# Optimization experiments

Measured on AMD Instinct MI355X. Metric: run time of the kernel, lower is better.

The kernel has to match this reference:

```python
import jax, jax.numpy as jnp
import numpy as np

# loss weights (match init_kwargs)
L_M, L_U, L_B, L_D = 1.0, 7.0, 2.0, 1.0
NV, NP, NI, NB = 500_000, 64, 48, 2  # voxels, predictions, instances, batches


def setup_inputs() -> dict:
    key = jax.random.key(0)
    k1, k2 = jax.random.split(key)
    logits = jax.random.normal(k1, (NV, NP), dtype=jnp.float32)
    # sorted batch ids per voxel (first half batch 0, second half batch 1)
    voxel_batch = (jnp.arange(NV) * NB // NV).astype(jnp.int32)
    per_b = NI // NB
    # instance ids consistent with voxel batch (module assumes one batch per instance)
    gt_ids = (voxel_batch * per_b + jax.random.randint(k2, (NV,), 0, per_b)).astype(jnp.int32)
    centroid_batches = (jnp.arange(NP) * NB // NP).astype(jnp.int32)
    return {"logits": logits, "voxel_batch": voxel_batch, "gt_ids": gt_ids,
            "centroid_batches": centroid_batches}


def linear_sum_assignment(cost):
    """Hungarian algorithm (e-maxx JV variant) on a small numpy cost matrix."""
    cost = np.asarray(cost, dtype=np.float64)
    transposed = cost.shape[0] > cost.shape[1]
    C = cost.T if transposed else cost
    n, m = C.shape
    u = np.zeros(n + 1); v = np.zeros(m + 1)
    p = np.zeros(m + 1, dtype=np.int64); way = np.zeros(m + 1, dtype=np.int64)
    for i in range(1, n + 1):
        p[0] = i; j0 = 0
        minv = np.full(m + 1, np.inf); used = np.zeros(m + 1, dtype=bool)
        while True:
            used[j0] = True
            i0 = p[j0]; j1 = 0; delta = np.inf
            for j in range(1, m + 1):
                if not used[j]:
                    cur = C[i0 - 1, j - 1] - u[i0] - v[j]
                    if cur < minv[j]:
                        minv[j] = cur; way[j] = j0
                    if minv[j] < delta:
                        delta = minv[j]; j1 = j
            for j in range(m + 1):
                if used[j]:
                    u[p[j]] += delta; v[j] -= delta
                else:
                    minv[j] -= delta
            j0 = j1
            if p[j0] == 0:
                break
        while j0:
            j1 = way[j0]; p[j0] = p[j1]; j0 = j1
    ans = np.zeros(n, dtype=np.int64)
    for j in range(1, m + 1):
        if p[j] > 0:
            ans[p[j] - 1] = j - 1
    rows, cols = np.arange(n), ans
    if transposed:
        rows, cols = cols, rows
    order = np.argsort(rows)
    return rows[order], cols[order]


def reference(logits, voxel_batch, gt_ids, centroid_batches):
    vb = np.asarray(voxel_batch); gi = np.asarray(gt_ids); cb = np.asarray(centroid_batches)
    batches = np.unique(vb)
    uniq, inv = np.unique(gi, return_inverse=True)
    uniq_batches = np.zeros(uniq.size, dtype=np.int64)
    uniq_batches[inv] = vb  # batch id per unique GT instance
    losses = jnp.zeros(5, dtype=logits.dtype)
    for b in batches:
        vox = np.nonzero(vb == b)[0]
        pidx = np.nonzero(cb == b)[0]
        gidx = np.nonzero(uniq_batches == b)[0]
        if pidx.size == 0:
            continue
        x = logits[jnp.asarray(vox)][:, jnp.asarray(pidx)].T          # [P, Nv_b]
        g = (jnp.asarray(gi[vox])[None, :] == jnp.asarray(uniq[gidx])[:, None]).astype(logits.dtype)  # [G, Nv_b]
        # matcher pairwise costs (mean BCE + dice)
        pos = jnp.logaddexp(0.0, -x)  # BCE(x, 1) per element
        neg = jnp.logaddexp(0.0, x)   # BCE(x, 0) per element
        nvb = x.shape[1]
        cost_bce = (pos @ g.T + neg @ (1.0 - g).T) / nvb              # [P, G]
        p = jax.nn.sigmoid(x)
        cost_dice = 1.0 - (2.0 * (p @ g.T) + 1.0) / (p.sum(1)[:, None] + g.sum(1)[None, :] + 1.0)
        cost = L_B * cost_bce + L_D * cost_dice
        pr, gr = linear_sum_assignment(np.asarray(cost))
        G = g.shape[0]
        xm = x[jnp.asarray(pr)]; gm = g[jnp.asarray(gr)]              # matched pairs
        bce = L_B * (jnp.logaddexp(0.0, xm) - xm * gm).mean(1).sum() / G
        pm = jax.nn.sigmoid(xm)
        dice = L_D * (1.0 - (2.0 * (pm * gm).sum(1) + 1.0) / (pm.sum(1) + gm.sum(1) + 1.0)).sum() / G
        matched = L_M * (bce + dice)
        um = np.setdiff1d(np.arange(x.shape[0]), pr)
        if um.size:
            xu = x[jnp.asarray(um)]
            pu = jax.nn.sigmoid(xu)
            # sigmoid focal loss vs zeros: alpha_t=0.75, (1-p_t)^2 = p^2, ce = softplus(x)
            unmatched = L_U * (0.75 * jnp.logaddexp(0.0, xu) * pu * pu).mean()
        else:
            unmatched = jnp.zeros((), logits.dtype)
        total = matched + unmatched
        losses = losses + jnp.stack([total, matched, unmatched, bce, dice])
    return losses / batches.size  # [total, matched, unmatched, bce, dice]
```

## Files before the change

### kernel.cpp

```cpp
#include <hip/hip_runtime.h>
#include <math.h>

#define PB 32
#define GB 24
#define NBUK 48
#define NH 256
#define SL 16
#define PART 160

__global__ __launch_bounds__(256) void k_hist(const int* __restrict__ gi, int NV,
                                              int* __restrict__ counts)
{
    __shared__ int h[NBUK];
    int t = threadIdx.x;
    if (t < NBUK) h[t] = 0;
    __syncthreads();
    int CH = (NV + NH - 1) / NH;
    int lo = blockIdx.x * CH, hi = lo + CH; if (hi > NV) hi = NV;
    for (int i = lo + t; i < hi; i += 256) atomicAdd(&h[gi[i]], 1);
    __syncthreads();
    if (t < NBUK) counts[t * NH + blockIdx.x] = h[t];
}

__global__ __launch_bounds__(1024) void k_scan(const int* __restrict__ counts,
                                               int* __restrict__ offs, int* __restrict__ bs)
{
    __shared__ int tot[NBUK];
    __shared__ int bstart[NBUK + 1];
    int t = threadIdx.x, w = t >> 6, lane = t & 63;
    int c[3][4]; int excl[3];
    #pragma unroll
    for (int q = 0; q < 3; ++q) {
        int g = w * 3 + q;
        int base = g * NH + lane * 4;
        int s = 0;
        #pragma unroll
        for (int j = 0; j < 4; ++j) { c[q][j] = counts[base + j]; s += c[q][j]; }
        int inc = s;
        for (int off = 1; off < 64; off <<= 1) {
            int v = __shfl_up(inc, off);
            if (lane >= off) inc += v;
        }
        excl[q] = inc - s;
        int rt = __shfl(inc, 63);
        if (lane == 0) tot[g] = rt;
    }
    __syncthreads();
    if (t == 0) {
        int acc = 0;
        for (int g = 0; g < NBUK; ++g) { bstart[g] = acc; acc += tot[g]; }
        bstart[NBUK] = acc;
        for (int g = 0; g <= NBUK; ++g) bs[g] = bstart[g];
    }
    __syncthreads();
    #pragma unroll
    for (int q = 0; q < 3; ++q) {
        int g = w * 3 + q;
        int run = excl[q] + bstart[g];
        #pragma unroll
        for (int j = 0; j < 4; ++j) { offs[g * NH + lane * 4 + j] = run; run += c[q][j]; }
    }
}

__global__ __launch_bounds__(256) void k_scatter(const int* __restrict__ gi, int NV,
                                                 const int* __restrict__ offs,
                                                 int* __restrict__ sidx)
{
    __shared__ int cur[NBUK];
    __shared__ int wcnt[4][NBUK];
    int t = threadIdx.x, w = t >> 6, lane = t & 63;
    if (t < NBUK) cur[t] = offs[t * NH + blockIdx.x];
    int CH = (NV + NH - 1) / NH;
    int lo = blockIdx.x * CH, hi = lo + CH; if (hi > NV) hi = NV;
    int qlo = (gi[lo] >= GB) ? GB : 0;
    int qhi = (gi[hi - 1] >= GB) ? NBUK : GB;
    unsigned long long below = (lane == 0) ? 0ull : ((~0ull) >> (64 - lane));

    for (int base = lo; base < hi; base += 256) {
        int v = base + t;
        bool act = (v < hi);
        int g = act ? gi[v] : -1;
        for (int j = t; j < 4 * NBUK; j += 256) (&wcnt[0][0])[j] = 0;
        __syncthreads();
        int rank_in_wave = 0;
        for (int q = qlo; q < qhi; ++q) {
            unsigned long long m = __ballot(g == q);
            if (m) {
                if (g == q) rank_in_wave = __popcll(m & below);
                if (lane == __ffsll((unsigned long long)m) - 1) wcnt[w][q] = __popcll(m);
            }
        }
        __syncthreads();
        if (act) {
            int pre = 0;
            for (int ww = 0; ww < w; ++ww) pre += wcnt[ww][g];
            sidx[cur[g] + pre + rank_in_wave] = v;
        }
        __syncthreads();
        if (t >= qlo && t < qhi) {
            int s = 0;
            for (int ww = 0; ww < 4; ++ww) s += wcnt[ww][t];
            cur[t] += s;
        }
        __syncthreads();
    }
}

__global__ __launch_bounds__(256) void k_accum2(
    const float* __restrict__ logits, const int* __restrict__ sidx,
    const int* __restrict__ bs, float* __restrict__ partials)
{
    int g = blockIdx.x >> 4, s = blockIdx.x & 15;
    int b = (g >= GB) ? 1 : 0;
    int lo = bs[g], hi = bs[g + 1];
    int sz = hi - lo;
    int sl = (sz + SL - 1) / SL;
    int p0 = lo + s * sl, p1 = p0 + sl; if (p1 > hi) p1 = hi;

    int t = threadIdx.x, w = t >> 6, lane = t & 63;
    int vi = lane >> 3, c0 = (lane & 7) * 4;
    int wn = p1 - p0;
    int wl = (wn + 3) / 4;
    int q0 = p0 + w * wl, q1 = q0 + wl; if (q1 > p1) q1 = p1;

    const float* xb = logits + 32 * b + c0;
    float sx[4] = {0,0,0,0}, sg[4] = {0,0,0,0};
    float tn[4] = {0,0,0,0}, ts[4] = {0,0,0,0}, tf[4] = {0,0,0,0};

    #pragma unroll 2
    for (int pos = q0; pos < q1; pos += 8) {
        int pv = pos + vi;
        if (pv < q1) {
            int idx = sidx[pv];
            float4 xq = *(const float4*)(xb + (size_t)idx * 64);
            float xs[4] = {xq.x, xq.y, xq.z, xq.w};
            #pragma unroll
            for (int e = 0; e < 4; ++e) {
                float x  = xs[e];
                float ax = fabsf(x);
                float ex = __expf(-ax);
                float neg = fmaxf(x, 0.f) + __logf(1.f + ex);
                float r  = __builtin_amdgcn_rcpf(1.f + ex);
                float sig = (x >= 0.f) ? r : ex * r;
                sx[e] += x;
                sg[e] += sig;
                tn[e] += neg;
                ts[e] += sig;
                tf[e] += neg * sig * sig;
            }
        }
    }

    #pragma unroll
    for (int off = 8; off <= 32; off <<= 1) {
        #pragma unroll
        for (int e = 0; e < 4; ++e) {
            sx[e] += __shfl_xor(sx[e], off);
            sg[e] += __shfl_xor(sg[e], off);
            tn[e] += __shfl_xor(tn[e], off);
            ts[e] += __shfl_xor(ts[e], off);
            tf[e] += __shfl_xor(tf[e], off);
        }
    }

    __shared__ float red[4][5][PB];
    if (lane < 8) {
        #pragma unroll
        for (int e = 0; e < 4; ++e) {
            red[w][0][c0 + e] = sx[e];
            red[w][1][c0 + e] = sg[e];
            red[w][2][c0 + e] = tn[e];
            red[w][3][c0 + e] = ts[e];
            red[w][4][c0 + e] = tf[e];
        }
    }
    __syncthreads();
    float* op = partials + (size_t)blockIdx.x * PART;
    for (int j = t; j < PART; j += 256)
        op[j] = (&red[0][0][0])[j] + (&red[1][0][0])[j] + (&red[2][0][0])[j] + (&red[3][0][0])[j];
}

#define DPPMIN(ctrl) { int tdp = __builtin_amdgcn_update_dpp(vbits, vbits, ctrl, 0xf, 0xf, false); \
    vbits = __float_as_int(fminf(__int_as_float(vbits), __int_as_float(tdp))); }
__device__ __forceinline__ float wave_min64(float x) {
    int vbits = __float_as_int(x);
    DPPMIN(0x111); DPPMIN(0x112); DPPMIN(0x114); DPPMIN(0x118);
    float a = __int_as_float(__builtin_amdgcn_readlane(vbits, 15));
    float b = __int_as_float(__builtin_amdgcn_readlane(vbits, 31));
    float c = __int_as_float(__builtin_amdgcn_readlane(vbits, 47));
    float d = __int_as_float(__builtin_amdgcn_readlane(vbits, 63));
    return fminf(fminf(a, b), fminf(c, d));
}

__global__ __launch_bounds__(1024) void k_final(
    const float* __restrict__ partials, const int* __restrict__ bs, float* __restrict__ outp)
{
    __shared__ float fs2[NBUK][5][PB];
    __shared__ float tneg[2][PB], tsig[2][PB], tfoc[2][PB];
    __shared__ float cntf[NBUK];
    __shared__ float nvbs[2];
    __shared__ float Ct[2][GB][PB];
    __shared__ float uincr[2][GB];
    __shared__ double bres[2][3];

    int tid = threadIdx.x;
    for (int j = tid; j < NBUK * PART; j += 1024) {
        int g = j / PART, r = j % PART;
        const float* base = partials + (size_t)g * SL * PART + r;
        float s = 0.f;
        #pragma unroll
        for (int k = 0; k < SL; ++k) s += base[(size_t)k * PART];
        (&fs2[0][0][0])[j] = s;
    }
    if (tid < NBUK) cntf[tid] = (float)(bs[tid + 1] - bs[tid]);
    __syncthreads();

    if (tid < 64) {
        int b = tid >> 5, p = tid & 31;
        float a = 0.f, c = 0.f, d = 0.f;
        for (int i = 0; i < GB; ++i) {
            a += fs2[b*GB + i][2][p];
            c += fs2[b*GB + i][3][p];
            d += fs2[b*GB + i][4][p];
        }
        tneg[b][p] = a; tsig[b][p] = c; tfoc[b][p] = d;
    }
    if (tid >= 64 && tid < 66) {
        int b = tid - 64; float s = 0.f;
        for (int i = 0; i < GB; ++i) s += cntf[b*GB + i];
        nvbs[b] = s;
    }
    __syncthreads();

    for (int idx = tid; idx < 2*GB*PB; idx += 1024) {
        int b = idx / (GB*PB), r = idx % (GB*PB), i = r / PB, j = r % PB;
        float nv = nvbs[b];
        float sx   = fs2[b*GB + i][0][j];
        float ssig = fs2[b*GB + i][1][j];
        float bceC  = 2.0f * (tneg[b][j] - sx) / nv;
        float diceC = 1.0f - (2.f*ssig + 1.f) / (tsig[b][j] + cntf[b*GB + i] + 1.f);
        Ct[b][i][j] = bceC + diceC;
    }
    __syncthreads();

    int wave = tid >> 6;
    int lane = tid & 63;
    if (tid < 128) {
        int b = wave;
        int j = lane;
        bool valid = (j >= 1 && j <= PB);
        float u_reg = 0.f;
        float v_reg = 0.f;
        int   p_reg = 0;

        for (int i = 1; i <= GB; ++i) {
            float Mv = 3e38f;
            int   way_reg = 0;
            bool  used = (lane == 0);
            float Duse = 0.f;
            if (lane == 0) p_reg = i;
            if (lane < GB) uincr[b][lane] = 0.f;
            int j0 = 0;
            float D = 0.f;
            int i0 = i;
            unsigned long long freecols =
                __ballot(p_reg == 0) & 0x1FFFFFFFEull;
            for (int it = 0; it < 2*PB + 4; ++it) {
                float u0 = __int_as_float(__builtin_amdgcn_readlane(__float_as_int(u_reg), i0 - 1));
                float Crow = valid ? Ct[b][i0-1][j-1] : 0.f;
                float cur = Crow - u0 - v_reg + D;
                if (valid && !used && cur < Mv) { Mv = cur; way_reg = j0; }
                float cand = (valid && !used) ? Mv : 3e38f;
                float dm = wave_min64(cand);
                unsigned long long msk = __ballot(cand == dm);
                int j1 = (int)__ffsll(msk) - 1;
                D = dm;
                if (lane == j1) { used = true; Duse = dm; }
                j0 = j1;
                if ((freecols >> j1) & 1) break;
                i0 = __builtin_amdgcn_readlane(p_reg, j1);
            }
            if (used) {
                v_reg -= (D - Duse);
                if (p_reg > 0) uincr[b][p_reg - 1] = D - Duse;
            }
            int jj = j0;
            for (int g2 = 0; g2 < PB + 2 && jj; ++g2) {
                int j1 = __builtin_amdgcn_readlane(way_reg, jj);
                int pj1 = __builtin_amdgcn_readlane(p_reg, j1);
                if (lane == jj) p_reg = pj1;
                jj = j1;
            }
            if (lane < GB) u_reg += uincr[b][lane];
        }

        double nvbd = (double)nvbs[b];
        double myb = 0.0, myd = 0.0, myf = 0.0, myu = 0.0;
        if (valid) {
            int pj = p_reg;
            int p = j - 1;
            if (pj > 0) {
                int ii = pj - 1;
                myb = ((double)tneg[b][p] - (double)fs2[b*GB + ii][0][p]) / nvbd;
                myd = 1.0 - (2.0*(double)fs2[b*GB + ii][1][p] + 1.0) /
                            ((double)tsig[b][p] + (double)cntf[b*GB + ii] + 1.0);
            } else {
                myf = (double)tfoc[b][p];
                myu = 1.0;
            }
        }
        #pragma unroll
        for (int off = 32; off >= 1; off >>= 1) {
            myb += __shfl_xor(myb, off);
            myd += __shfl_xor(myd, off);
            myf += __shfl_xor(myf, off);
            myu += __shfl_xor(myu, off);
        }
        if (lane == 0) {
            double G = (double)GB;
            double bce  = 2.0 * myb / G;
            double dice = 1.0 * myd / G;
            double unm  = (myu > 0.0) ? 7.0 * 0.75 * myf / (myu * nvbd)
                                      : 0.0;
            bres[b][0] = bce; bres[b][1] = dice; bres[b][2] = unm;
        }
    }
    __syncthreads();

    if (tid == 0) {
        double L[5] = {0,0,0,0,0};
        for (int b = 0; b < 2; ++b) {
            double bce = bres[b][0], dice = bres[b][1], unm = bres[b][2];
            double matched = bce + dice;
            double total = matched + unm;
            L[0] += total; L[1] += matched; L[2] += unm; L[3] += bce; L[4] += dice;
        }
        for (int k2 = 0; k2 < 5; ++k2) outp[k2] = (float)(L[k2] / 2.0);
    }
}

extern "C" void kernel_launch(void* const* d_in, const int* in_sizes, int n_in,
                              void* d_out, int out_size, void* d_ws, size_t ws_size,
                              hipStream_t stream)
{
    const float* logits = (const float*)d_in[0];
    const int* gi = (const int*)d_in[2];
    int NV = in_sizes[1];

    int* wsi = (int*)d_ws;
    int* counts = wsi;
    int* offs   = counts + NBUK * NH;
    int* bs     = offs + NBUK * NH;
    int* sidx   = bs + 64;
    float* partials = (float*)(sidx + NV);

    hipLaunchKernelGGL(k_hist,    dim3(NH), dim3(256), 0, stream, gi, NV, counts);
    hipLaunchKernelGGL(k_scan,    dim3(1), dim3(1024), 0, stream, counts, offs, bs);
    hipLaunchKernelGGL(k_scatter, dim3(NH), dim3(256), 0, stream, gi, NV, offs, sidx);
    hipLaunchKernelGGL(k_accum2,  dim3(NBUK * SL), dim3(256), 0, stream, logits, sidx, bs, partials);
    hipLaunchKernelGGL(k_final,   dim3(1), dim3(1024), 0, stream, partials, bs, (float*)d_out);
}
```

Before: 106.5 us.

## Split final kernel into staging kernel and register-resident Hungarian solver

The single 1024-thread final kernel is split in two. One kernel reduces the partials and writes the cost matrix and auxiliary sums to a workspace buffer. A separate 128-thread kernel loads each lane's cost column into 24 registers and selects rows with a branch-free select tree instead of reading shared memory on every augmentation step. This is meant to shorten the serial Hungarian loop's per-iteration latency and to avoid running it with a 1024-thread launch bound. It adds an extra kernel launch and a global-memory round trip for the staged data.

Result: slower. 136.6 us (+28.3%).

```diff
diff --git a/kernel.cpp b/kernel.cpp
--- a/kernel.cpp
+++ b/kernel.cpp
@@ -7,6 +7,16 @@
 #define NH 256
 #define SL 16
 #define PART 160
+
+#define SB_CT 0
+#define SB_SX 1536
+#define SB_SS 3072
+#define SB_TN 4608
+#define SB_TS 4672
+#define SB_TF 4736
+#define SB_CNT 4800
+#define SB_NVB 4848
+#define SB_SZ 4864
 
 __global__ __launch_bounds__(256) void k_hist(const int* __restrict__ gi, int NV,
                                               int* __restrict__ counts)
@@ -180,6 +190,63 @@
         op[j] = (&red[0][0][0])[j] + (&red[1][0][0])[j] + (&red[2][0][0])[j] + (&red[3][0][0])[j];
 }
 
+__global__ __launch_bounds__(1024) void k_stage(
+    const float* __restrict__ partials, const int* __restrict__ bs, float* __restrict__ sb)
+{
+    __shared__ float fs2[NBUK][5][PB];
+    __shared__ float tneg[2][PB], tsig[2][PB], tfoc[2][PB];
+    __shared__ float cntf[NBUK];
+    __shared__ float nvbs[2];
+
+    int tid = threadIdx.x;
+    for (int j = tid; j < NBUK * PART; j += 1024) {
+        int g = j / PART, r = j % PART;
+        const float* base = partials + (size_t)g * SL * PART + r;
+        float s = 0.f;
+        #pragma unroll
+        for (int k = 0; k < SL; ++k) s += base[(size_t)k * PART];
+        (&fs2[0][0][0])[j] = s;
+    }
+    if (tid < NBUK) cntf[tid] = (float)(bs[tid + 1] - bs[tid]);
+    __syncthreads();
+
+    if (tid < 64) {
+        int b = tid >> 5, p = tid & 31;
+        float a = 0.f, c = 0.f, d = 0.f;
+        for (int i = 0; i < GB; ++i) {
+            a += fs2[b*GB + i][2][p];
+            c += fs2[b*GB + i][3][p];
+            d += fs2[b*GB + i][4][p];
+        }
+        tneg[b][p] = a; tsig[b][p] = c; tfoc[b][p] = d;
+    }
+    if (tid >= 64 && tid < 66) {
+        int b = tid - 64; float s = 0.f;
+        for (int i = 0; i < GB; ++i) s += cntf[b*GB + i];
+        nvbs[b] = s;
+    }
+    __syncthreads();
+
+    for (int idx = tid; idx < 2*GB*PB; idx += 1024) {
+        int b = idx / (GB*PB), r = idx % (GB*PB), i = r / PB, j = r % PB;
+        float nv = nvbs[b];
+        float sx   = fs2[b*GB + i][0][j];
+        float ssig = fs2[b*GB + i][1][j];
+        float bceC  = 2.0f * (tneg[b][j] - sx) / nv;
+        float diceC = 1.0f - (2.f*ssig + 1.f) / (tsig[b][j] + cntf[b*GB + i] + 1.f);
+        sb[SB_CT + idx] = bceC + diceC;
+        sb[SB_SX + idx] = sx;
+        sb[SB_SS + idx] = ssig;
+    }
+    if (tid < 64) {
+        sb[SB_TN + tid] = tneg[tid >> 5][tid & 31];
+        sb[SB_TS + tid] = tsig[tid >> 5][tid & 31];
+        sb[SB_TF + tid] = tfoc[tid >> 5][tid & 31];
+    }
+    if (tid >= 64 && tid < 64 + NBUK) sb[SB_CNT + tid - 64] = cntf[tid - 64];
+    if (tid >= 128 && tid < 130) sb[SB_NVB + tid - 128] = nvbs[tid - 128];
+}
+
 #define DPPMIN(ctrl) { int tdp = __builtin_amdgcn_update_dpp(vbits, vbits, ctrl, 0xf, 0xf, false); \
     vbits = __float_as_int(fminf(__int_as_float(vbits), __int_as_float(tdp))); }
 __device__ __forceinline__ float wave_min64(float x) {
@@ -192,145 +259,123 @@
     return fminf(fminf(a, b), fminf(c, d));
 }
 
-__global__ __launch_bounds__(1024) void k_final(
-    const float* __restrict__ partials, const int* __restrict__ bs, float* __restrict__ outp)
-{
-    __shared__ float fs2[NBUK][5][PB];
-    __shared__ float tneg[2][PB], tsig[2][PB], tfoc[2][PB];
-    __shared__ float cntf[NBUK];
-    __shared__ float nvbs[2];
-    __shared__ float Ct[2][GB][PB];
+__device__ __forceinline__ float sel24(const float (&c)[GB], int k) {
+    float a[12];
+    #pragma unroll
+    for (int i = 0; i < 12; ++i) a[i] = (k & 1) ? c[2*i+1] : c[2*i];
+    float b2[6];
+    #pragma unroll
+    for (int i = 0; i < 6; ++i) b2[i] = (k & 2) ? a[2*i+1] : a[2*i];
+    float d[3];
+    #pragma unroll
+    for (int i = 0; i < 3; ++i) d[i] = (k & 4) ? b2[2*i+1] : b2[2*i];
+    float e0 = (k & 8) ? d[1] : d[0];
+    return (k & 16) ? d[2] : e0;
+}
+
+__global__ __launch_bounds__(128) void k_jv(const float* __restrict__ sb, float* __restrict__ outp)
+{
     __shared__ float uincr[2][GB];
     __shared__ double bres[2][3];
 
     int tid = threadIdx.x;
-    for (int j = tid; j < NBUK * PART; j += 1024) {
-        int g = j / PART, r = j % PART;
-        const float* base = partials + (size_t)g * SL * PART + r;
-        float s = 0.f;
-        #pragma unroll
-        for (int k = 0; k < SL; ++k) s += base[(size_t)k * PART];
-        (&fs2[0][0][0])[j] = s;
-    }
-    if (tid < NBUK) cntf[tid] = (float)(bs[tid + 1] - bs[tid]);
-    __syncthreads();
-
-    if (tid < 64) {
-        int b = tid >> 5, p = tid & 31;
-        float a = 0.f, c = 0.f, d = 0.f;
-        for (int i = 0; i < GB; ++i) {
-            a += fs2[b*GB + i][2][p];
-            c += fs2[b*GB + i][3][p];
-            d += fs2[b*GB + i][4][p];
-        }
-        tneg[b][p] = a; tsig[b][p] = c; tfoc[b][p] = d;
-    }
-    if (tid >= 64 && tid < 66) {
-        int b = tid - 64; float s = 0.f;
-        for (int i = 0; i < GB; ++i) s += cntf[b*GB + i];
-        nvbs[b] = s;
-    }
-    __syncthreads();
-
-    for (int idx = tid; idx < 2*GB*PB; idx += 1024) {
-        int b = idx / (GB*PB), r = idx % (GB*PB), i = r / PB, j = r % PB;
-        float nv = nvbs[b];
-        float sx   = fs2[b*GB + i][0][j];
-        float ssig = fs2[b*GB + i][1][j];
-        float bceC  = 2.0f * (tneg[b][j] - sx) / nv;
-        float diceC = 1.0f - (2.f*ssig + 1.f) / (tsig[b][j] + cntf[b*GB + i] + 1.f);
-        Ct[b][i][j] = bceC + diceC;
-    }
-    __syncthreads();
-
-    int wave = tid >> 6;
-    int lane = tid & 63;
-    if (tid < 128) {
-        int b = wave;
-        int j = lane;
-        bool valid = (j >= 1 && j <= PB);
-        float u_reg = 0.f;
-        float v_reg = 0.f;
-        int   p_reg = 0;
-
-        for (int i = 1; i <= GB; ++i) {
-            float Mv = 3e38f;
-            int   way_reg = 0;
-            bool  used = (lane == 0);
-            float Duse = 0.f;
-            if (lane == 0) p_reg = i;
-            if (lane < GB) uincr[b][lane] = 0.f;
-            int j0 = 0;
-            float D = 0.f;
-            int i0 = i;
-            unsigned long long freecols =
-                __ballot(p_reg == 0) & 0x1FFFFFFFEull;
-            for (int it = 0; it < 2*PB + 4; ++it) {
-                float u0 = __int_as_float(__builtin_amdgcn_readlane(__float_as_int(u_reg), i0 - 1));
-                float Crow = valid ? Ct[b][i0-1][j-1] : 0.f;
-                float cur = Crow - u0 - v_reg + D;
-                if (valid && !used && cur < Mv) { Mv = cur; way_reg = j0; }
-                float cand = (valid && !used) ? Mv : 3e38f;
-                float dm = wave_min64(cand);
-                unsigned long long msk = __ballot(cand == dm);
-                int j1 = (int)__ffsll(msk) - 1;
-                D = dm;
-                if (lane == j1) { used = true; Duse = dm; }
-                j0 = j1;
-                if ((freecols >> j1) & 1) break;
-                i0 = __builtin_amdgcn_readlane(p_reg, j1);
-            }
-            if (used) {
-                v_reg -= (D - Duse);
-                if (p_reg > 0) uincr[b][p_reg - 1] = D - Duse;
-            }
-            int jj = j0;
-            for (int g2 = 0; g2 < PB + 2 && jj; ++g2) {
-                int j1 = __builtin_amdgcn_readlane(way_reg, jj);
-                int pj1 = __builtin_amdgcn_readlane(p_reg, j1);
-                if (lane == jj) p_reg = pj1;
-                jj = j1;
-            }
-            if (lane < GB) u_reg += uincr[b][lane];
-        }
-
-        double nvbd = (double)nvbs[b];
-        double myb = 0.0, myd = 0.0, myf = 0.0, myu = 0.0;
-        if (valid) {
-            int pj = p_reg;
-            int p = j - 1;
-            if (pj > 0) {
-                int ii = pj - 1;
-                myb = ((double)tneg[b][p] - (double)fs2[b*GB + ii][0][p]) / nvbd;
-                myd = 1.0 - (2.0*(double)fs2[b*GB + ii][1][p] + 1.0) /
-                            ((double)tsig[b][p] + (double)cntf[b*GB + ii] + 1.0);
-            } else {
-                myf = (double)tfoc[b][p];
-                myu = 1.0;
-            }
-        }
-        #pragma unroll
-        for (int off = 32; off >= 1; off >>= 1) {
-            myb += __shfl_xor(myb, off);
-            myd += __shfl_xor(myd, off);
-            myf += __shfl_xor(myf, off);
-            myu += __shfl_xor(myu, off);
-        }
-        if (lane == 0) {
-            double G = (double)GB;
-            double bce  = 2.0 * myb / G;
-            double dice = 1.0 * myd / G;
-            double unm  = (myu > 0.0) ? 7.0 * 0.75 * myf / (myu * nvbd)
-                                      : 0.0;
-            bres[b][0] = bce; bres[b][1] = dice; bres[b][2] = unm;
-        }
+    int b = tid >> 6, lane = tid & 63;
+    int j = lane;
+    bool valid = (j >= 1 && j <= PB);
+
+    float creg[GB];
+    #pragma unroll
+    for (int i = 0; i < GB; ++i)
+        creg[i] = valid ? sb[SB_CT + b*GB*PB + i*PB + (j-1)] : 0.f;
+    float tn_p = valid ? sb[SB_TN + b*PB + (j-1)] : 0.f;
+    float ts_p = valid ? sb[SB_TS + b*PB + (j-1)] : 0.f;
+    float tf_p = valid ? sb[SB_TF + b*PB + (j-1)] : 0.f;
+    float nvb  = sb[SB_NVB + b];
+
+    float u_reg = 0.f;
+    float v_reg = 0.f;
+    int   p_reg = 0;
+
+    for (int i = 1; i <= GB; ++i) {
+        float Mv = 3e38f;
+        int   way_reg = 0;
+        bool  used = (lane == 0);
+        float Duse = 0.f;
+        if (lane == 0) p_reg = i;
+        if (lane < GB) uincr[b][lane] = 0.f;
+        int j0 = 0;
+        float D = 0.f;
+        int i0 = i;
+        unsigned long long freecols =
+            __ballot(p_reg == 0) & 0x1FFFFFFFEull;
+        for (int it = 0; it < 2*PB + 4; ++it) {
+            float u0 = __int_as_float(__builtin_amdgcn_readlane(__float_as_int(u_reg), i0 - 1));
+            float Crow = sel24(creg, i0 - 1);
+            float cur = Crow - u0 - v_reg + D;
+            if (valid && !used && cur < Mv) { Mv = cur; way_reg = j0; }
+            float cand = (valid && !used) ? Mv : 3e38f;
+            float dm = wave_min64(cand);
+            unsigned long long msk = __ballot(cand == dm);
+            int j1 = (int)__ffsll(msk) - 1;
+            D = dm;
+            if (lane == j1) { used = true; Duse = dm; }
+            j0 = j1;
+            if ((freecols >> j1) & 1) break;
+            i0 = __builtin_amdgcn_readlane(p_reg, j1);
+        }
+        if (used) {
+            v_reg -= (D - Duse);
+            if (p_reg > 0) uincr[b][p_reg - 1] = D - Duse;
+        }
+        int jj = j0;
+        for (int g2 = 0; g2 < PB + 2 && jj; ++g2) {
+            int j1 = __builtin_amdgcn_readlane(way_reg, jj);
+            int pj1 = __builtin_amdgcn_readlane(p_reg, j1);
+            if (lane == jj) p_reg = pj1;
+            jj = j1;
+        }
+        if (lane < GB) u_reg += uincr[b][lane];
+    }
+
+    double nvbd = (double)nvb;
+    double myb = 0.0, myd = 0.0, myf = 0.0, myu = 0.0;
+    if (valid) {
+        int pj = p_reg;
+        int p = j - 1;
+        if (pj > 0) {
+            int ii = pj - 1;
+            float sxv = sb[SB_SX + b*GB*PB + ii*PB + p];
+            float ssv = sb[SB_SS + b*GB*PB + ii*PB + p];
+            float cnv = sb[SB_CNT + b*GB + ii];
+            myb = ((double)tn_p - (double)sxv) / nvbd;
+            myd = 1.0 - (2.0*(double)ssv + 1.0) /
+                        ((double)ts_p + (double)cnv + 1.0);
+        } else {
+            myf = (double)tf_p;
+            myu = 1.0;
+        }
+    }
+    #pragma unroll
+    for (int off = 32; off >= 1; off >>= 1) {
+        myb += __shfl_xor(myb, off);
+        myd += __shfl_xor(myd, off);
+        myf += __shfl_xor(myf, off);
+        myu += __shfl_xor(myu, off);
+    }
+    if (lane == 0) {
+        double G = (double)GB;
+        double bce  = 2.0 * myb / G;
+        double dice = 1.0 * myd / G;
+        double unm  = (myu > 0.0) ? 7.0 * 0.75 * myf / (myu * nvbd)
+                                  : 0.0;
+        bres[b][0] = bce; bres[b][1] = dice; bres[b][2] = unm;
     }
     __syncthreads();
 
     if (tid == 0) {
         double L[5] = {0,0,0,0,0};
-        for (int b = 0; b < 2; ++b) {
-            double bce = bres[b][0], dice = bres[b][1], unm = bres[b][2];
+        for (int bb = 0; bb < 2; ++bb) {
+            double bce = bres[bb][0], dice = bres[bb][1], unm = bres[bb][2];
             double matched = bce + dice;
             double total = matched + unm;
             L[0] += total; L[1] += matched; L[2] += unm; L[3] += bce; L[4] += dice;
@@ -353,10 +398,12 @@
     int* bs     = offs + NBUK * NH;
     int* sidx   = bs + 64;
     float* partials = (float*)(sidx + NV);
+    float* sb       = partials + NBUK * SL * PART;
 
     hipLaunchKernelGGL(k_hist,    dim3(NH), dim3(256), 0, stream, gi, NV, counts);
     hipLaunchKernelGGL(k_scan,    dim3(1), dim3(1024), 0, stream, counts, offs, bs);
     hipLaunchKernelGGL(k_scatter, dim3(NH), dim3(256), 0, stream, gi, NV, offs, sidx);
     hipLaunchKernelGGL(k_accum2,  dim3(NBUK * SL), dim3(256), 0, stream, logits, sidx, bs, partials);
-    hipLaunchKernelGGL(k_final,   dim3(1), dim3(1024), 0, stream, partials, bs, (float*)d_out);
-}
+    hipLaunchKernelGGL(k_stage,   dim3(1), dim3(1024), 0, stream, partials, bs, sb);
+    hipLaunchKernelGGL(k_jv,      dim3(1), dim3(128), 0, stream, sb, (float*)d_out);
+}
```
